# Performance work log

Hardware: AMD Instinct MI355X
Metric: run time of the kernel (lower is better)

Reference implementation:

```python
import jax, jax.numpy as jnp
import numpy as np

# Integration setup: torch code integrates t in [0,1] with dopri5.
# We use the dopri5 (RK45) Butcher tableau with a fixed step count so the
# reference is deterministic and jit/vjp friendly; per-stage math is identical.
N_STEPS = 16
T0, T1 = 0.0, 1.0

# dopri5 tableau
C2, C3, C4, C5, C6 = 1/5, 3/10, 4/5, 8/9, 1.0
A21 = 1/5
A31, A32 = 3/40, 9/40
A41, A42, A43 = 44/45, -56/15, 32/9
A51, A52, A53, A54 = 19372/6561, -25360/2187, 64448/6561, -212/729
A61, A62, A63, A64, A65 = 9017/3168, -355/33, 46732/5247, 49/176, -5103/18656
B1, B3, B4, B5, B6 = 35/384, 500/1113, 125/192, -2187/6784, 11/84  # 5th-order weights (b2=b7=0)


def setup_inputs() -> dict:
    key = jax.random.key(0)
    k0, k1, k2, k3 = jax.random.split(key, 4)
    B, D, H = 16384, 256, 512
    x = jax.random.normal(k0, (B, D), jnp.float32)
    W1 = jax.random.normal(k1, (D, H), jnp.float32) / np.sqrt(D).astype(np.float32)
    b1 = jnp.zeros((H,), jnp.float32)
    W2 = jax.random.normal(k2, (H, D), jnp.float32) / np.sqrt(H).astype(np.float32)
    b2 = jnp.zeros((D,), jnp.float32)
    Wfc = jax.random.normal(k3, (D, 1), jnp.float32) / np.sqrt(D).astype(np.float32)
    bfc = jnp.zeros((1,), jnp.float32)
    return {"x": x, "W1": W1, "b1": b1, "W2": W2, "b2": b2, "Wfc": Wfc, "bfc": bfc}


def reference(x, W1, b1, W2, b2, Wfc, bfc):
    def f(t, y):  # autonomous MLP vector field: dim -> hidden -> dim
        return jnp.tanh(y @ W1 + b1) @ W2 + b2

    dt = jnp.float32((T1 - T0) / N_STEPS)

    def step(carry, _):
        t, y = carry
        k1 = f(t, y)
        k2 = f(t + C2 * dt, y + dt * (A21 * k1))
        k3 = f(t + C3 * dt, y + dt * (A31 * k1 + A32 * k2))
        k4 = f(t + C4 * dt, y + dt * (A41 * k1 + A42 * k2 + A43 * k3))
        k5 = f(t + C5 * dt, y + dt * (A51 * k1 + A52 * k2 + A53 * k3 + A54 * k4))
        k6 = f(t + C6 * dt, y + dt * (A61 * k1 + A62 * k2 + A63 * k3 + A64 * k4 + A65 * k5))
        y_next = y + dt * (B1 * k1 + B3 * k3 + B4 * k4 + B5 * k5 + B6 * k6)
        return (t + dt, y_next), None

    (_, y1), _ = jax.lax.scan(step, (jnp.float32(T0), x), None, length=N_STEPS)
    return y1 @ Wfc + bfc  # [B, 1]
```

## Files before the change

### kernel.cpp

```cpp
#include <hip/hip_runtime.h>

typedef unsigned short u16;
typedef unsigned int   u32;
typedef __bf16 bf16x8 __attribute__((ext_vector_type(8)));
typedef float  f32x4  __attribute__((ext_vector_type(4)));
typedef u32    u32x2  __attribute__((ext_vector_type(2)));

#define DIMD  256
#define DIMH  512
#define MTILE 64
#define NTHREADS 512

#define USTR 264
#define HSTR 520
#define U_BASE 0
#define H_BASE (MTILE*USTR)
#define LDS_U16 (H_BASE + MTILE*HSTR)

#define DT 0.0625f

__device__ __forceinline__ u16 f2bf(float f) {
  u32 u = __float_as_uint(f);
  u += 0x7FFFu + ((u >> 16) & 1u);
  return (u16)(u >> 16);
}
__device__ __forceinline__ u32 pk(float a, float b) {
#if __has_builtin(__builtin_amdgcn_cvt_pk_bf16_f32)
  auto v = __builtin_amdgcn_cvt_pk_bf16_f32(a, b);
  u32 r; __builtin_memcpy(&r, &v, 4); return r;
#else
  return (u32)f2bf(a) | ((u32)f2bf(b) << 16);
#endif
}
__device__ __forceinline__ float bflo(u32 p) { return __uint_as_float(p << 16); }
__device__ __forceinline__ float bfhi(u32 p) { return __uint_as_float(p & 0xFFFF0000u); }
__device__ __forceinline__ float tanh_fast(float x) {
  float e = __builtin_amdgcn_exp2f(x * 2.8853900817779268f);
  return 1.0f - 2.0f * __builtin_amdgcn_rcpf(e + 1.0f);
}

__device__ __forceinline__ void bar_lds() {
  asm volatile("" ::: "memory");
  __builtin_amdgcn_s_waitcnt(0xC07F);
  __builtin_amdgcn_s_barrier();
  asm volatile("" ::: "memory");
}

__global__ void convert_w(const float* __restrict__ W1, const float* __restrict__ W2,
                          u16* __restrict__ w1t, u16* __restrict__ w2t) {
  int idx = blockIdx.x * 256 + threadIdx.x;
  {
    int n = idx >> 8, k = idx & 255;
    w1t[idx] = f2bf(W1[k * DIMH + n]);
  }
  {
    int n = idx >> 9, k = idx & 511;
    w2t[idx] = f2bf(W2[k * DIMD + n]);
  }
}

__device__ __forceinline__ void mfma_16(f32x4 (&acc)[4][4],
                                        const bf16x8 (&a)[4], const bf16x8 (&b)[4]) {
#pragma unroll
  for (int mb = 0; mb < 4; ++mb)
#pragma unroll
    for (int nb = 0; nb < 4; ++nb)
      acc[mb][nb] = __builtin_amdgcn_mfma_f32_16x16x32_bf16(a[mb], b[nb], acc[mb][nb], 0, 0, 0);
}
__device__ __forceinline__ void mfma_8(f32x4 (&acc)[2][4],
                                       const bf16x8 (&a)[2], const bf16x8 (&b)[4]) {
#pragma unroll
  for (int mb = 0; mb < 2; ++mb)
#pragma unroll
    for (int nb = 0; nb < 4; ++nb)
      acc[mb][nb] = __builtin_amdgcn_mfma_f32_16x16x32_bf16(a[mb], b[nb], acc[mb][nb], 0, 0, 0);
}

__global__ __attribute__((amdgpu_flat_work_group_size(NTHREADS, NTHREADS),
                          amdgpu_waves_per_eu(2, 2)))
void ode_fused(
    const float* __restrict__ x,   const float* __restrict__ b1,
    const float* __restrict__ b2,  const float* __restrict__ wfc,
    const float* __restrict__ bfc, const u16* __restrict__ w1t,
    const u16* __restrict__ w2t,   float* __restrict__ out)
{
  __shared__ u16 lds[LDS_U16];
  __shared__ u32 k2f[16 * NTHREADS];

  const int tid   = threadIdx.x;
  const int wg    = blockIdx.x;
  const int wv    = tid >> 6;
  const int lane  = tid & 63;
  const int lanel = lane & 15;
  const int laneq = lane >> 4;

  const u16* uRd = &lds[U_BASE + lanel * USTR + laneq * 8];
  const u16* hRd = &lds[H_BASE + lanel * HSTR + laneq * 8];
  u16* uWr = &lds[U_BASE + lanel * USTR + wv * 32 + laneq * 4];
  u16* hWr = &lds[H_BASE + lanel * HSTR + wv * 64 + laneq * 4];


  u32 b1p[8], b2p[4];
#pragma unroll
  for (int mb = 0; mb < 4; ++mb) {
    int base = wv * 64 + mb * 16 + laneq * 4;
    b1p[mb * 2 + 0] = pk(b1[base + 0], b1[base + 1]);
    b1p[mb * 2 + 1] = pk(b1[base + 2], b1[base + 3]);
  }
#pragma unroll
  for (int mb = 0; mb < 2; ++mb) {
    int base = wv * 32 + mb * 16 + laneq * 4;
    b2p[mb * 2 + 0] = pk(b2[base + 0], b2[base + 1]);
    b2p[mb * 2 + 1] = pk(b2[base + 2], b2[base + 3]);
  }

  float yv[32];
#pragma unroll
  for (int nb = 0; nb < 4; ++nb)
#pragma unroll
    for (int mb = 0; mb < 2; ++mb) {
      const float4 v = *(const float4*)&x[(wg * 64 + nb * 16 + lanel) * DIMD +
                                          wv * 32 + mb * 16 + laneq * 4];
      int i = nb * 8 + mb * 4;
      yv[i + 0] = v.x; yv[i + 1] = v.y; yv[i + 2] = v.z; yv[i + 3] = v.w;
    }

#pragma unroll
  for (int nb = 0; nb < 4; ++nb)
#pragma unroll
    for (int mb = 0; mb < 2; ++mb) {
      int i = nb * 8 + mb * 4;
      u32x2 w; w.x = pk(yv[i], yv[i + 1]); w.y = pk(yv[i + 2], yv[i + 3]);
      *(u32x2*)(uWr + nb * 16 * USTR + mb * 16) = w;
    }

  const u16* w1base[4];
#pragma unroll
  for (int mb = 0; mb < 4; ++mb)
    w1base[mb] = w1t + (wv * 64 + mb * 16 + lanel) * DIMD + laneq * 8;
  const u16* w2base[2];
#pragma unroll
  for (int mb = 0; mb < 2; ++mb)
    w2base[mb] = w2t + (wv * 32 + mb * 16 + lanel) * DIMH + laneq * 8;

  auto ldA1 = [&](bf16x8 (&a)[4], int kk) {
#pragma unroll
    for (int mb = 0; mb < 4; ++mb) a[mb] = *(const bf16x8*)(w1base[mb] + kk * 32);
  };
  auto ldB1 = [&](bf16x8 (&b)[4], int kk) {
#pragma unroll
    for (int nb = 0; nb < 4; ++nb) b[nb] = *(const bf16x8*)(uRd + nb * 16 * USTR + kk * 32);
  };
  auto ldA2 = [&](bf16x8 (&a)[2], int kk) {
#pragma unroll
    for (int mb = 0; mb < 2; ++mb) a[mb] = *(const bf16x8*)(w2base[mb] + kk * 32);
  };
  auto ldB2 = [&](bf16x8 (&b)[4], int kk) {
#pragma unroll
    for (int nb = 0; nb < 4; ++nb) b[nb] = *(const bf16x8*)(hRd + nb * 16 * HSTR + kk * 32);
  };

  u32 st[32];

  bf16x8 aP1[4];
  ldA1(aP1, 0);
  bar_lds();

#pragma unroll 1
  for (int step = 0; step < 16; ++step) {
#pragma unroll 1
    for (int s = 1; s <= 6; ++s) {
      f32x4 acc[4][4];
#pragma unroll
      for (int mb = 0; mb < 4; ++mb)
#pragma unroll
        for (int nb = 0; nb < 4; ++nb) acc[mb][nb] = (f32x4){0.f, 0.f, 0.f, 0.f};
      bf16x8 aA[4], bA[4], aB[4], bB[4];
#pragma unroll
      for (int mb = 0; mb < 4; ++mb) aA[mb] = aP1[mb];
      ldB1(bA, 0);
#pragma unroll 1
      for (int kk2 = 0; kk2 < 3; ++kk2) {
        ldA1(aB, 2 * kk2 + 1); ldB1(bB, 2 * kk2 + 1);
        mfma_16(acc, aA, bA);
        ldA1(aA, 2 * kk2 + 2); ldB1(bA, 2 * kk2 + 2);
        mfma_16(acc, aB, bB);
      }
      ldA1(aB, 7); ldB1(bB, 7);
      mfma_16(acc, aA, bA);
      bf16x8 aP2[2];
      ldA2(aP2, 0);
      mfma_16(acc, aB, bB);

#pragma unroll
      for (int mb = 0; mb < 4; ++mb)
#pragma unroll
        for (int nb = 0; nb < 4; ++nb) {
          float h0 = tanh_fast(acc[mb][nb][0] + bflo(b1p[mb * 2 + 0]));
          float h1 = tanh_fast(acc[mb][nb][1] + bfhi(b1p[mb * 2 + 0]));
          float h2 = tanh_fast(acc[mb][nb][2] + bflo(b1p[mb * 2 + 1]));
          float h3 = tanh_fast(acc[mb][nb][3] + bfhi(b1p[mb * 2 + 1]));
          u32x2 w; w.x = pk(h0, h1); w.y = pk(h2, h3);
          *(u32x2*)(hWr + nb * 16 * HSTR + mb * 16) = w;
        }
      bar_lds();

      f32x4 acc2[2][4];
#pragma unroll
      for (int mb = 0; mb < 2; ++mb)
#pragma unroll
        for (int nb = 0; nb < 4; ++nb) acc2[mb][nb] = (f32x4){0.f, 0.f, 0.f, 0.f};
      bf16x8 cA[2], dA[4], cB[2], dB[4];
#pragma unroll
      for (int mb = 0; mb < 2; ++mb) cA[mb] = aP2[mb];
      ldB2(dA, 0);
#pragma unroll 1
      for (int kk2 = 0; kk2 < 7; ++kk2) {
        ldA2(cB, 2 * kk2 + 1); ldB2(dB, 2 * kk2 + 1);
        mfma_8(acc2, cA, dA);
        ldA2(cA, 2 * kk2 + 2); ldB2(dA, 2 * kk2 + 2);
        mfma_8(acc2, cB, dB);
      }
      ldA2(cB, 15); ldB2(dB, 15);
      mfma_8(acc2, cA, dA);
      ldA1(aP1, 0);
      mfma_8(acc2, cB, dB);

      if (s == 1) {
        const float C = DT * 0.2f;
#pragma unroll
        for (int mb = 0; mb < 2; ++mb)
#pragma unroll
          for (int nb = 0; nb < 4; ++nb) {
            int i = nb * 8 + mb * 4, p = nb * 4 + mb * 2;
            float k0 = acc2[mb][nb][0] + bflo(b2p[mb * 2 + 0]);
            float k1 = acc2[mb][nb][1] + bfhi(b2p[mb * 2 + 0]);
            float k2 = acc2[mb][nb][2] + bflo(b2p[mb * 2 + 1]);
            float k3 = acc2[mb][nb][3] + bfhi(b2p[mb * 2 + 1]);
            st[p] = pk(k0, k1); st[p + 1] = pk(k2, k3);
            u32x2 w;
            w.x = pk(yv[i] + C * k0, yv[i + 1] + C * k1);
            w.y = pk(yv[i + 2] + C * k2, yv[i + 3] + C * k3);
            *(u32x2*)(uWr + nb * 16 * USTR + mb * 16) = w;
          }
      } else if (s == 2) {
        const float C1 = DT * 0.075f, C2 = DT * 0.225f;
#pragma unroll
        for (int mb = 0; mb < 2; ++mb)
#pragma unroll
          for (int nb = 0; nb < 4; ++nb) {
            int i = nb * 8 + mb * 4, p = nb * 4 + mb * 2;
            float k0 = acc2[mb][nb][0] + bflo(b2p[mb * 2 + 0]);
            float k1 = acc2[mb][nb][1] + bfhi(b2p[mb * 2 + 0]);
            float k2 = acc2[mb][nb][2] + bflo(b2p[mb * 2 + 1]);
            float k3 = acc2[mb][nb][3] + bfhi(b2p[mb * 2 + 1]);
            k2f[p * NTHREADS + tid]       = pk(k0, k1);
            k2f[(p + 1) * NTHREADS + tid] = pk(k2, k3);
            u32x2 w;
            w.x = pk(yv[i]     + C1 * bflo(st[p])     + C2 * k0,
                     yv[i + 1] + C1 * bfhi(st[p])     + C2 * k1);
            w.y = pk(yv[i + 2] + C1 * bflo(st[p + 1]) + C2 * k2,
                     yv[i + 3] + C1 * bfhi(st[p + 1]) + C2 * k3);
            *(u32x2*)(uWr + nb * 16 * USTR + mb * 16) = w;
          }
      } else if (s == 3) {
        const float C1 = DT * (float)(44.0/45.0);
        const float C2 = DT * (float)(-56.0/15.0);
        const float C3 = DT * (float)(32.0/9.0);
#pragma unroll
        for (int mb = 0; mb < 2; ++mb)
#pragma unroll
          for (int nb = 0; nb < 4; ++nb) {
            int i = nb * 8 + mb * 4, p = nb * 4 + mb * 2;
            float k0 = acc2[mb][nb][0] + bflo(b2p[mb * 2 + 0]);
            float k1 = acc2[mb][nb][1] + bfhi(b2p[mb * 2 + 0]);
            float k2 = acc2[mb][nb][2] + bflo(b2p[mb * 2 + 1]);
            float k3 = acc2[mb][nb][3] + bfhi(b2p[mb * 2 + 1]);
            st[16 + p] = pk(k0, k1); st[16 + p + 1] = pk(k2, k3);
            u32 q0 = k2f[p * NTHREADS + tid], q1 = k2f[(p + 1) * NTHREADS + tid];
            u32x2 w;
            w.x = pk(yv[i]     + C1 * bflo(st[p])     + C2 * bflo(q0) + C3 * k0,
                     yv[i + 1] + C1 * bfhi(st[p])     + C2 * bfhi(q0) + C3 * k1);
            w.y = pk(yv[i + 2] + C1 * bflo(st[p + 1]) + C2 * bflo(q1) + C3 * k2,
                     yv[i + 3] + C1 * bfhi(st[p + 1]) + C2 * bfhi(q1) + C3 * k3);
            *(u32x2*)(uWr + nb * 16 * USTR + mb * 16) = w;
          }
      } else if (s == 4) {
        const float C51 = DT * (float)(19372.0/6561.0);
        const float C52 = DT * (float)(-25360.0/2187.0);
        const float C53 = DT * (float)(64448.0/6561.0);
        const float C54 = DT * (float)(-212.0/729.0);
        const float D61 = DT * (float)(9017.0/3168.0  - 35.0/384.0);
        const float D62 = DT * (float)(-355.0/33.0);
        const float D63 = DT * (float)(46732.0/5247.0 - 500.0/1113.0);
        const float D64 = DT * (float)(49.0/176.0     - 125.0/192.0);
        const float E1  = DT * (float)(35.0/384.0);
        const float E3  = DT * (float)(500.0/1113.0);
        const float E4  = DT * (float)(125.0/192.0);
#pragma unroll
        for (int mb = 0; mb < 2; ++mb)
#pragma unroll
          for (int nb = 0; nb < 4; ++nb) {
            int i = nb * 8 + mb * 4, p = nb * 4 + mb * 2;
            float k40 = acc2[mb][nb][0] + bflo(b2p[mb * 2 + 0]);
            float k41 = acc2[mb][nb][1] + bfhi(b2p[mb * 2 + 0]);
            float k42 = acc2[mb][nb][2] + bflo(b2p[mb * 2 + 1]);
            float k43 = acc2[mb][nb][3] + bfhi(b2p[mb * 2 + 1]);
            float k10 = bflo(st[p]),      k11 = bfhi(st[p]);
            float k12 = bflo(st[p + 1]),  k13 = bfhi(st[p + 1]);
            u32 q0 = k2f[p * NTHREADS + tid], q1 = k2f[(p + 1) * NTHREADS + tid];
            float k20 = bflo(q0), k21 = bfhi(q0);
            float k22 = bflo(q1), k23 = bfhi(q1);
            float k30 = bflo(st[16 + p]),     k31 = bfhi(st[16 + p]);
            float k32 = bflo(st[16 + p + 1]), k33 = bfhi(st[16 + p + 1]);
            u32x2 w;
            w.x = pk(yv[i]     + C51 * k10 + C52 * k20 + C53 * k30 + C54 * k40,
                     yv[i + 1] + C51 * k11 + C52 * k21 + C53 * k31 + C54 * k41);
            w.y = pk(yv[i + 2] + C51 * k12 + C52 * k22 + C53 * k32 + C54 * k42,
                     yv[i + 3] + C51 * k13 + C52 * k23 + C53 * k33 + C54 * k43);
            *(u32x2*)(uWr + nb * 16 * USTR + mb * 16) = w;
            st[p]     = pk(D61 * k10 + D62 * k20 + D63 * k30 + D64 * k40,
                           D61 * k11 + D62 * k21 + D63 * k31 + D64 * k41);
            st[p + 1] = pk(D61 * k12 + D62 * k22 + D63 * k32 + D64 * k42,
                           D61 * k13 + D62 * k23 + D63 * k33 + D64 * k43);
            yv[i]     += E1 * k10 + E3 * k30 + E4 * k40;
            yv[i + 1] += E1 * k11 + E3 * k31 + E4 * k41;
            yv[i + 2] += E1 * k12 + E3 * k32 + E4 * k42;
            yv[i + 3] += E1 * k13 + E3 * k33 + E4 * k43;
          }
      } else if (s == 5) {
        const float D65 = DT * (float)(-5103.0/18656.0 + 2187.0/6784.0);
        const float E5  = DT * (float)(-2187.0/6784.0);
#pragma unroll
        for (int mb = 0; mb < 2; ++mb)
#pragma unroll
          for (int nb = 0; nb < 4; ++nb) {
            int i = nb * 8 + mb * 4, p = nb * 4 + mb * 2;
            float k0 = acc2[mb][nb][0] + bflo(b2p[mb * 2 + 0]);
            float k1 = acc2[mb][nb][1] + bfhi(b2p[mb * 2 + 0]);
            float k2 = acc2[mb][nb][2] + bflo(b2p[mb * 2 + 1]);
            float k3 = acc2[mb][nb][3] + bfhi(b2p[mb * 2 + 1]);
            u32x2 w;
            w.x = pk(yv[i]     + bflo(st[p])     + D65 * k0,
                     yv[i + 1] + bfhi(st[p])     + D65 * k1);
            w.y = pk(yv[i + 2] + bflo(st[p + 1]) + D65 * k2,
                     yv[i + 3] + bfhi(st[p + 1]) + D65 * k3);
            *(u32x2*)(uWr + nb * 16 * USTR + mb * 16) = w;
            yv[i]     += E5 * k0;
            yv[i + 1] += E5 * k1;
            yv[i + 2] += E5 * k2;
            yv[i + 3] += E5 * k3;
          }
      } else {
        const float E6 = DT * (float)(11.0/84.0);
#pragma unroll
        for (int mb = 0; mb < 2; ++mb)
#pragma unroll
          for (int nb = 0; nb < 4; ++nb) {
            int i = nb * 8 + mb * 4;
            yv[i]     += E6 * (acc2[mb][nb][0] + bflo(b2p[mb * 2 + 0]));
            yv[i + 1] += E6 * (acc2[mb][nb][1] + bfhi(b2p[mb * 2 + 0]));
            yv[i + 2] += E6 * (acc2[mb][nb][2] + bflo(b2p[mb * 2 + 1]));
            yv[i + 3] += E6 * (acc2[mb][nb][3] + bfhi(b2p[mb * 2 + 1]));
            u32x2 w;
            w.x = pk(yv[i], yv[i + 1]); w.y = pk(yv[i + 2], yv[i + 3]);
            *(u32x2*)(uWr + nb * 16 * USTR + mb * 16) = w;
          }
      }
      bar_lds();
    }
  }

  {
    float wfcv[8];
#pragma unroll
    for (int mb = 0; mb < 2; ++mb)
#pragma unroll
      for (int r = 0; r < 4; ++r)
        wfcv[mb * 4 + r] = wfc[wv * 32 + mb * 16 + laneq * 4 + r];
    float* redf = (float*)lds;
    float pr[4];
#pragma unroll
    for (int nb = 0; nb < 4; ++nb) {
      float p = 0.f;
#pragma unroll
      for (int mb = 0; mb < 2; ++mb)
#pragma unroll
        for (int r = 0; r < 4; ++r)
          p += yv[nb * 8 + mb * 4 + r] * wfcv[mb * 4 + r];
      p += __shfl_xor(p, 16);
      p += __shfl_xor(p, 32);
      pr[nb] = p;
    }
    if (laneq == 0) {
#pragma unroll
      for (int nb = 0; nb < 4; ++nb)
        redf[(nb * 16 + lanel) * 8 + wv] = pr[nb];
    }
    __syncthreads();
    if (tid < 64) {
      float s = bfc[0];
#pragma unroll
      for (int w = 0; w < 8; ++w) s += redf[tid * 8 + w];
      out[wg * 64 + tid] = s;
    }
  }
}

extern "C" void kernel_launch(void* const* d_in, const int* in_sizes, int n_in,
                              void* d_out, int out_size, void* d_ws, size_t ws_size,
                              hipStream_t stream) {
  const float* x   = (const float*)d_in[0];
  const float* W1  = (const float*)d_in[1];
  const float* b1  = (const float*)d_in[2];
  const float* W2  = (const float*)d_in[3];
  const float* b2  = (const float*)d_in[4];
  const float* wfc = (const float*)d_in[5];
  const float* bfc = (const float*)d_in[6];
  float* out = (float*)d_out;

  u16* w1t = (u16*)d_ws;
  u16* w2t = w1t + DIMH * DIMD;

  hipLaunchKernelGGL(convert_w, dim3(512), dim3(256), 0, stream, W1, W2, w1t, w2t);
  hipLaunchKernelGGL(ode_fused, dim3(16384 / MTILE), dim3(NTHREADS), 0, stream,
                     x, b1, b2, wfc, bfc, w1t, w2t, out);
}
```

Baseline: 1.625 ms.

## Split tanh epilogue and overlap second half with GEMM2 even k-steps

Writes only the first half of the hidden tile (mb 0-1) to LDS before the barrier. The second half's tanh and LDS stores now run while the second GEMM processes even k-blocks, which depend only on the first half. A second barrier follows before the odd k-blocks. The aim is to hide the tanh/pack epilogue latency behind MFMA work, at the cost of an extra barrier and a less sequential access order.

```diff
diff --git a/kernel.cpp b/kernel.cpp
--- a/kernel.cpp
+++ b/kernel.cpp
@@ -193,7 +193,7 @@
       mfma_16(acc, aB, bB);
 
 #pragma unroll
-      for (int mb = 0; mb < 4; ++mb)
+      for (int mb = 0; mb < 2; ++mb)
 #pragma unroll
         for (int nb = 0; nb < 4; ++nb) {
           float h0 = tanh_fast(acc[mb][nb][0] + bflo(b1p[mb * 2 + 0]));
@@ -214,11 +214,38 @@
 #pragma unroll
       for (int mb = 0; mb < 2; ++mb) cA[mb] = aP2[mb];
       ldB2(dA, 0);
+
+#pragma unroll
+      for (int mb = 2; mb < 4; ++mb)
+#pragma unroll
+        for (int nb = 0; nb < 4; ++nb) {
+          float h0 = tanh_fast(acc[mb][nb][0] + bflo(b1p[mb * 2 + 0]));
+          float h1 = tanh_fast(acc[mb][nb][1] + bfhi(b1p[mb * 2 + 0]));
+          float h2 = tanh_fast(acc[mb][nb][2] + bflo(b1p[mb * 2 + 1]));
+          float h3 = tanh_fast(acc[mb][nb][3] + bfhi(b1p[mb * 2 + 1]));
+          u32x2 w; w.x = pk(h0, h1); w.y = pk(h2, h3);
+          *(u32x2*)(hWr + nb * 16 * HSTR + mb * 16) = w;
+        }
+
 #pragma unroll 1
-      for (int kk2 = 0; kk2 < 7; ++kk2) {
-        ldA2(cB, 2 * kk2 + 1); ldB2(dB, 2 * kk2 + 1);
+      for (int j = 0; j < 3; ++j) {
+        ldA2(cB, 4 * j + 2); ldB2(dB, 4 * j + 2);
         mfma_8(acc2, cA, dA);
-        ldA2(cA, 2 * kk2 + 2); ldB2(dA, 2 * kk2 + 2);
+        ldA2(cA, 4 * j + 4); ldB2(dA, 4 * j + 4);
+        mfma_8(acc2, cB, dB);
+      }
+      ldA2(cB, 14); ldB2(dB, 14);
+      mfma_8(acc2, cA, dA);
+      ldA2(cA, 1);
+      mfma_8(acc2, cB, dB);
+      bar_lds();
+
+      ldB2(dA, 1);
+#pragma unroll 1
+      for (int j = 0; j < 3; ++j) {
+        ldA2(cB, 4 * j + 3); ldB2(dB, 4 * j + 3);
+        mfma_8(acc2, cA, dA);
+        ldA2(cA, 4 * j + 5); ldB2(dA, 4 * j + 5);
         mfma_8(acc2, cB, dB);
       }
       ldA2(cB, 15); ldB2(dB, 15);
```

Measured after the change: 1.606 ms. About the same (-1.2%).
